# Kernel optimization log

Measured on AMD Instinct MI355X. Metric: run time of the kernel, lower is better.

The kernel has to match this reference:

```python
import jax, jax.numpy as jnp
import numpy as np

D = 768   # embedding_dimensions (richness) — hardcoded in source
H = 3     # heads — hardcoded in source


def setup_inputs() -> dict:
    key = jax.random.key(0)
    ks = jax.random.split(key, 12)
    s = 1.0 / np.sqrt(D)
    s3 = 1.0 / np.sqrt(H * D)
    return {
        "x": jax.random.normal(ks[0], (4, 2048, D), dtype=jnp.float32),
        # QKV projections: Linear(D, D*H), stored as (in, out)
        "Wq": jax.random.uniform(ks[1], (D, D * H), jnp.float32, -s, s),
        "bq": jax.random.uniform(ks[2], (D * H,), jnp.float32, -s, s),
        "Wk": jax.random.uniform(ks[3], (D, D * H), jnp.float32, -s, s),
        "bk": jax.random.uniform(ks[4], (D * H,), jnp.float32, -s, s),
        "Wv": jax.random.uniform(ks[5], (D, D * H), jnp.float32, -s, s),
        "bv": jax.random.uniform(ks[6], (D * H,), jnp.float32, -s, s),
        # final projection: Linear(H*D, D)
        "Wo": jax.random.uniform(ks[7], (H * D, D), jnp.float32, -s3, s3),
        "bo": jax.random.uniform(ks[8], (D,), jnp.float32, -s3, s3),
        # FFN: Linear(D, D) + LeakyReLU
        "Wf": jax.random.uniform(ks[9], (D, D), jnp.float32, -s, s),
        "bf": jax.random.uniform(ks[10], (D,), jnp.float32, -s, s),
    }


def reference(x, Wq, bq, Wk, bk, Wv, bv, Wo, bo, Wf, bf):
    B, S, _ = x.shape
    # QKV: [B,S,H*D] -> [B,H,S,D]  (head dim == full D, as in source)
    q = (x @ Wq + bq).reshape(B, S, H, D).transpose(0, 2, 1, 3)
    k = (x @ Wk + bk).reshape(B, S, H, D).transpose(0, 2, 1, 3)
    v = (x @ Wv + bv).reshape(B, S, H, D).transpose(0, 2, 1, 3)
    # unscaled attention scores (source applies no 1/sqrt(d))
    scores = jnp.einsum('bhqd,bhkd->bhqk', q, k)
    # faithful masking: tril of the scores themselves, fill zeros with -99999
    masked = jnp.where(jnp.tril(scores) == 0, jnp.float32(-99999.0), scores)
    attn = jax.nn.softmax(masked, axis=-1)
    o = jnp.einsum('bhqk,bhkd->bhqd', attn, v)
    o = o.transpose(0, 2, 1, 3).reshape(B, S, H * D)
    a = o @ Wo + bo
    # "normalisation": subtract global mean over the whole tensor
    n = a - jnp.mean(a)
    y = n + x  # residual
    return jax.nn.leaky_relu(y @ Wf + bf, negative_slope=0.01)
```

## Files before the change

kernel.cpp:

```cpp
#include <hip/hip_runtime.h>
#include <hip/hip_bf16.h>

typedef __attribute__((ext_vector_type(8))) __bf16 bf16x8;
typedef __attribute__((ext_vector_type(4))) float f32x4;
typedef unsigned short u16;

#define DEV static __device__ __forceinline__

#define BAR() asm volatile("s_barrier" ::: "memory")
#define LGKM0() asm volatile("s_waitcnt lgkmcnt(0)" ::: "memory")
#define VMCNT6() asm volatile("s_waitcnt vmcnt(6)" ::: "memory")
#define VMCNT3() asm volatile("s_waitcnt vmcnt(3)" ::: "memory")
#define VMCNT0() asm volatile("s_waitcnt vmcnt(0)" ::: "memory")

DEV void load_lds16(const void* g, void* l) {
  __builtin_amdgcn_global_load_lds(
      (const __attribute__((address_space(1))) unsigned int*)g,
      (__attribute__((address_space(3))) unsigned int*)l, 16, 0, 0);
}

DEV u16 bf16bits(float v) {
  __hip_bfloat16 h = __float2bfloat16(v);
  return __builtin_bit_cast(u16, h);
}

DEV bf16x8 rdfrag(const u16* region, int row, int ks, int l) {
  const int cb = (((ks << 6) | ((l >> 4) << 4)) ^ ((l & 7) << 4));
  return *(const bf16x8*)((const char*)region + row * 128 + cb);
}

DEV bf16x8 rdfrag32(const u16* region, int row, int l) {
  const int cb = (((l >> 4) ^ ((row >> 1) & 3)) << 4);
  return *(const bf16x8*)((const char*)region + row * 64 + cb);
}

struct OffN { unsigned long long a[12], b[12], c[12]; };

enum { G128_SC = 0, G128_PV = 1, G128_PLAIN = 2, G128_LEAKY = 3 };

__global__ __launch_bounds__(512, 1) void k_qkv256(
    const u16* __restrict__ A, const u16* __restrict__ B,
    const float* __restrict__ bias, u16* __restrict__ C, u16* __restrict__ Vt)
{
  int flat = blockIdx.y * 27 + blockIdx.x;
  flat = (flat & 7) * 108 + (flat >> 3);
  const int n0 = (flat % 27) * 256, m0 = (flat / 27) * 256;
  const int lda = 768, ldb = 768, nkt = 12;

  __shared__ u16 smem[65536];

  const int tid = threadIdx.x;
  const int l = tid & 63;
  const int wid = tid >> 6;
  const int wm = wid >> 1, wn = wid & 1;

  const int r0s = wid * 16 + (l >> 3);
  const int ces = ((l & 7) ^ (l >> 3)) << 3;
  const size_t aR0 = (size_t)(m0 + r0s) * lda + ces;
  const size_t aR1 = aR0 + (size_t)8 * lda;
  const size_t bR0 = (size_t)(n0 + r0s) * ldb + ces;
  const size_t bR1 = bR0 + (size_t)8 * ldb;
  const size_t hA = (size_t)128 * lda, hB = (size_t)128 * ldb;
  const int dst0 = wid * 1024 + l * 8, dst1 = dst0 + 512;
  u16* As0 = smem;
  u16* Bs0 = smem + 32768;

#define STAGE_A(bf, h, kkv) do {                                 \
    u16* Lp = As0 + (bf) * 16384 + (h) * 8192;                   \
    load_lds16(A + aR0 + ((h) ? hA : 0) + (kkv), Lp + dst0);     \
    load_lds16(A + aR1 + ((h) ? hA : 0) + (kkv), Lp + dst1);     \
  } while (0)
#define STAGE_B(bf, h, kkv) do {                                 \
    u16* Lp = Bs0 + (bf) * 16384 + (h) * 8192;                   \
    load_lds16(B + bR0 + ((h) ? hB : 0) + (kkv), Lp + dst0);     \
    load_lds16(B + bR1 + ((h) ? hB : 0) + (kkv), Lp + dst1);     \
  } while (0)

  f32x4 acc[2][2][2][4] = {};
  bf16x8 af[2][2], bA[4][2], bB[4][2];

#define MFMA16(QM, QN, BARR)                                                  \
    __builtin_amdgcn_s_setprio(1);                                            \
    _Pragma("unroll") for (int ks = 0; ks < 2; ks++)                          \
      _Pragma("unroll") for (int fm = 0; fm < 2; fm++)                        \
        _Pragma("unroll") for (int fn = 0; fn < 4; fn++)                      \
          acc[QM][QN][fm][fn] = __builtin_amdgcn_mfma_f32_16x16x32_bf16(      \
              af[fm][ks], BARR[fn][ks], acc[QM][QN][fm][fn], 0, 0, 0);        \
    __builtin_amdgcn_s_setprio(0);

#define RD_A(half)                                                            \
    _Pragma("unroll") for (int fm = 0; fm < 2; fm++)                          \
      _Pragma("unroll") for (int ks = 0; ks < 2; ks++)                        \
        af[fm][ks] = rdfrag(half, wm * 32 + fm * 16 + (l & 15), ks, l);
#define RD_B(dstv, half)                                                      \
    _Pragma("unroll") for (int fn = 0; fn < 4; fn++)                          \
      _Pragma("unroll") for (int ks = 0; ks < 2; ks++)                        \
        dstv[fn][ks] = rdfrag(half, wn * 64 + fn * 16 + (l & 15), ks, l);

  STAGE_A(0, 0, 0); STAGE_B(0, 0, 0); STAGE_B(0, 1, 0); STAGE_A(0, 1, 0);
  STAGE_A(1, 0, 64); STAGE_B(1, 0, 64); STAGE_B(1, 1, 64);
  VMCNT6();
  BAR();

  for (int t = 0; t < nkt; ++t) {
    const int cur = t & 1, nxt = cur ^ 1;
    const int kk1 = (t + 1) << 6, kk2 = (t + 2) << 6;
    const bool s1 = (t + 1 < nkt), s2 = (t + 2 < nkt);
    RD_A(As0 + cur * 16384);
    RD_B(bA, Bs0 + cur * 16384);
    if (s1) STAGE_A(nxt, 1, kk1);
    BAR();
    MFMA16(0, 0, bA);
    BAR();
    RD_B(bB, Bs0 + cur * 16384 + 8192);
    if (s2) STAGE_A(cur, 0, kk2);
    BAR();
    MFMA16(0, 1, bB);
    BAR();
    RD_A(As0 + cur * 16384 + 8192);
    if (s2) STAGE_B(cur, 0, kk2);
    BAR();
    MFMA16(1, 1, bB);
    BAR();
    if (s2) STAGE_B(cur, 1, kk2);
    BAR();
    MFMA16(1, 0, bA);
    if (s2) { VMCNT6(); } else { VMCNT0(); }
    BAR();
  }
#undef RD_A
#undef RD_B
#undef MFMA16
#undef STAGE_A
#undef STAGE_B

  __syncthreads();
  const int sel = n0 >= 4608 ? 2 : (n0 >= 2304 ? 1 : 0);
  const int r0c = (l >> 4) << 2;
  if (sel == 2) {
#pragma unroll
    for (int Qm = 0; Qm < 2; Qm++)
#pragma unroll
      for (int Qn = 0; Qn < 2; Qn++)
#pragma unroll
        for (int fn = 0; fn < 4; fn++) {
          const int coll = Qn * 128 + wn * 64 + fn * 16 + (l & 15);
          const float bv = bias[n0 + coll];
#pragma unroll
          for (int fm = 0; fm < 2; fm++)
#pragma unroll
            for (int r = 0; r < 4; r++) {
              const int rowl = Qm * 128 + wm * 32 + fm * 16 + r0c + r;
              smem[coll * 256 + ((((rowl >> 3) ^ (coll & 7)) << 3) | (rowl & 7))] =
                  bf16bits(acc[Qm][Qn][fm][fn][r] + bv);
            }
        }
    __syncthreads();
    const int n0v = n0 - 4608;
    const int h = n0v / 768, d0l = n0v % 768;
    const int b = m0 >> 11, sbase = m0 & 2047;
    u16* Cb = Vt + ((size_t)(b * 3 + h) * 768 + d0l) * 2048 + sbase;
#pragma unroll
    for (int j = 0; j < 16; j++) {
      const int dr = j * 16 + (tid >> 5);
      const int c8 = tid & 31;
      bf16x8 v = *(const bf16x8*)&smem[dr * 256 + ((c8 ^ (dr & 7)) << 3)];
      *(bf16x8*)&Cb[(size_t)dr * 2048 + c8 * 8] = v;
    }
  } else {
#pragma unroll
    for (int Qm = 0; Qm < 2; Qm++)
#pragma unroll
      for (int Qn = 0; Qn < 2; Qn++)
#pragma unroll
        for (int fn = 0; fn < 4; fn++) {
          const int coll = Qn * 128 + wn * 64 + fn * 16 + (l & 15);
          const float bv = bias[n0 + coll];
#pragma unroll
          for (int fm = 0; fm < 2; fm++)
#pragma unroll
            for (int r = 0; r < 4; r++) {
              const int rowl = Qm * 128 + wm * 32 + fm * 16 + r0c + r;
              smem[rowl * 256 + (coll ^ (((rowl >> 2) & 3) << 4))] =
                  bf16bits(acc[Qm][Qn][fm][fn][r] + bv);
            }
        }
    __syncthreads();
    u16* Cb = C + (size_t)sel * (8192ull * 2304) + (n0 - sel * 2304);
#pragma unroll
    for (int j = 0; j < 16; j++) {
      const int rowl = j * 16 + (tid >> 5);
      const int c = (tid & 31) * 8;
      bf16x8 v = *(const bf16x8*)&smem[rowl * 256 + (c ^ (((rowl >> 2) & 3) << 4))];
      *(bf16x8*)&Cb[(size_t)(m0 + rowl) * 2304 + c] = v;
    }
  }
}

template<int MODE>
__global__ __launch_bounds__(512, 4) void k_g128(
    const u16* __restrict__ Abase, const u16* __restrict__ Bbase,
    const float* __restrict__ bias, void* __restrict__ Cbase,
    float* __restrict__ part,
    long lda, long ldb, long ldc, int K, OffN off)
{
  int m0, n0, z, r = 0, rb = 0, nkt, arow0, brow0;
  const u16 *A, *B;
  if (MODE == G128_SC) {
    r = blockIdx.y; z = blockIdx.z;
    rb = r >> 1;
    if ((int)blockIdx.x > rb) return;
    m0 = r * 128; n0 = blockIdx.x * 256;
    nkt = K >> 5;
    A = Abase + off.a[z]; B = Bbase + off.b[z];
    arow0 = m0; brow0 = n0;
  } else if (MODE == G128_PV) {
    r = 15 - (int)blockIdx.y;
    rb = r >> 1;
    z = blockIdx.x / 3;
    m0 = r * 128; n0 = (blockIdx.x % 3) * 256;
    nkt = (rb + 1) * 8;
    lda = (long)(rb + 1) * 256;
    A = Abase + off.a[z] + (size_t)32768 * rb * (rb + 1);
    B = Bbase + off.b[z];
    arow0 = (r & 1) * 128; brow0 = n0;
  } else {
    z = 0;
    m0 = blockIdx.y * 128; n0 = blockIdx.x * 256;
    nkt = K >> 5;
    A = Abase; B = Bbase;
    arow0 = m0; brow0 = n0;
  }

  __shared__ u16 smem[39168];

  const int tid = threadIdx.x;
  const int l = tid & 63;
  const int wid = tid >> 6;
  const int wm = wid & 1;
  const int wn = wid >> 1;

  const int ces = (((tid & 3) ^ ((tid >> 3) & 3)) << 3);
  const u16* aS  = A + (size_t)(arow0 + (tid >> 2)) * lda + ces;
  const u16* bS0 = B + (size_t)(brow0 + (tid >> 2)) * ldb + ces;
  const u16* bS1 = bS0 + (size_t)128 * ldb;
  const int t8 = tid * 8;

#define STG(buf, kkv) do {                         \
    u16* Lp = smem + (buf) * 12288;                \
    load_lds16(aS + (kkv), Lp + t8);               \
    load_lds16(bS0 + (kkv), Lp + 4096 + t8);       \
    load_lds16(bS1 + (kkv), Lp + 8192 + t8);       \
  } while (0)

  float* ftab = (float*)(smem + 36864);
  if (MODE == G128_PV) {
    if (tid < 128) {
      const float2* pp = (const float2*)part + (size_t)z * 16384 + (m0 + tid);
      float m = -1e30f;
      for (int t = 0; t <= rb; t++) m = fmaxf(m, pp[(size_t)t * 2048].x);
      float den = 0.f;
      for (int t = 0; t <= rb; t++) {
        const float2 q = pp[(size_t)t * 2048];
        const float e = __expf(q.x - m);
        den += q.y * e;
        ftab[tid * 9 + t] = e;
      }
      ftab[tid * 9 + 8] = 1.f / den;
    }
    LGKM0();
  }

  f32x4 acc[4][4] = {};
  bf16x8 af[4], bf[4];

  STG(0, 0);
  STG(1, 32);
  VMCNT3();
  BAR();

  for (int t = 0; t < nkt; ++t) {
    const u16* Ar = smem + (t % 3) * 12288;
    const u16* Br = Ar + 4096;
#pragma unroll
    for (int fm = 0; fm < 4; fm++)
      af[fm] = rdfrag32(Ar, wm * 64 + fm * 16 + (l & 15), l);
#pragma unroll
    for (int fn = 0; fn < 4; fn++)
      bf[fn] = rdfrag32(Br, wn * 64 + fn * 16 + (l & 15), l);
    if (MODE == G128_PV) {
      const int tcol = t >> 3;
#pragma unroll
      for (int fm = 0; fm < 4; fm++) {
        const int row = wm * 64 + fm * 16 + (l & 15);
        const float ft = ftab[row * 9 + tcol];
#pragma unroll
        for (int i = 0; i < 8; i++)
          af[fm][i] = (__bf16)((float)af[fm][i] * ft);
      }
    }
    const bool s2 = (t + 2 < nkt);
    if (s2) STG((t + 2) % 3, (t + 2) << 5);
    __builtin_amdgcn_s_setprio(1);
#pragma unroll
    for (int fm = 0; fm < 4; fm++)
#pragma unroll
      for (int fn = 0; fn < 4; fn++)
        acc[fm][fn] = __builtin_amdgcn_mfma_f32_16x16x32_bf16(
            af[fm], bf[fn], acc[fm][fn], 0, 0, 0);
    __builtin_amdgcn_s_setprio(0);
    if (s2) { VMCNT3(); } else if (t + 1 < nkt) { VMCNT0(); }
    BAR();
  }
#undef STG

  const int r0c = (l >> 4) << 2;
  if (MODE == G128_SC) {
    float mx4[4][4], s4[4][4];
#pragma unroll
    for (int fm = 0; fm < 4; fm++)
#pragma unroll
      for (int rr = 0; rr < 4; rr++) {
        const int gi = m0 + wm * 64 + fm * 16 + r0c + rr;
        float mv = -1e30f;
#pragma unroll
        for (int fn = 0; fn < 4; fn++) {
          const int gc = n0 + wn * 64 + fn * 16 + (l & 15);
          float v = (gc <= gi) ? acc[fm][fn][rr] : -1e30f;
          acc[fm][fn][rr] = v;
          mv = fmaxf(mv, v);
        }
        mx4[fm][rr] = mv;
      }
#pragma unroll
    for (int o = 1; o < 16; o <<= 1)
#pragma unroll
      for (int fm = 0; fm < 4; fm++)
#pragma unroll
        for (int rr = 0; rr < 4; rr++)
          mx4[fm][rr] = fmaxf(mx4[fm][rr], __shfl_xor(mx4[fm][rr], o, 64));
    float* redm = (float*)smem;
    float* reds = redm + 512;
#pragma unroll
    for (int fm = 0; fm < 4; fm++)
#pragma unroll
      for (int rr = 0; rr < 4; rr++)
        if ((l & 15) == fm * 4 + rr)
          redm[(wm * 64 + fm * 16 + r0c + rr) * 4 + wn] = mx4[fm][rr];
    __syncthreads();
#pragma unroll
    for (int fm = 0; fm < 4; fm++)
#pragma unroll
      for (int rr = 0; rr < 4; rr++) {
        const int rowl = wm * 64 + fm * 16 + r0c + rr;
        f32x4 rm = *(const f32x4*)&redm[rowl * 4];
        const float tm = fmaxf(fmaxf(rm[0], rm[1]), fmaxf(rm[2], rm[3]));
        float ss = 0.f;
#pragma unroll
        for (int fn = 0; fn < 4; fn++) {
          const float e = __expf(acc[fm][fn][rr] - tm);
          acc[fm][fn][rr] = e;
          ss += e;
        }
        s4[fm][rr] = ss;
      }
#pragma unroll
    for (int o = 1; o < 16; o <<= 1)
#pragma unroll
      for (int fm = 0; fm < 4; fm++)
#pragma unroll
        for (int rr = 0; rr < 4; rr++)
          s4[fm][rr] += __shfl_xor(s4[fm][rr], o, 64);
#pragma unroll
    for (int fm = 0; fm < 4; fm++)
#pragma unroll
      for (int rr = 0; rr < 4; rr++)
        if ((l & 15) == fm * 4 + rr)
          reds[(wm * 64 + fm * 16 + r0c + rr) * 4 + wn] = s4[fm][rr];
    __syncthreads();
    if (tid < 128) {
      f32x4 rm = *(const f32x4*)&redm[tid * 4];
      f32x4 rs = *(const f32x4*)&reds[tid * 4];
      float2 pw;
      pw.x = fmaxf(fmaxf(rm[0], rm[1]), fmaxf(rm[2], rm[3]));
      pw.y = rs[0] + rs[1] + rs[2] + rs[3];
      ((float2*)part)[((size_t)z * 8 + blockIdx.x) * 2048 + m0 + tid] = pw;
    }
    __syncthreads();
#pragma unroll
    for (int fn = 0; fn < 4; fn++) {
      const int coll = wn * 64 + fn * 16 + (l & 15);
#pragma unroll
      for (int fm = 0; fm < 4; fm++)
#pragma unroll
        for (int rr = 0; rr < 4; rr++) {
          const int rowl = wm * 64 + fm * 16 + r0c + rr;
          smem[rowl * 256 + (coll ^ (((rowl >> 2) & 3) << 4))] =
              bf16bits(acc[fm][fn][rr]);
        }
    }
    __syncthreads();
    u16* Cb = (u16*)Cbase + off.c[z] + (size_t)32768 * rb * (rb + 1);
    const int W = (rb + 1) << 8;
    const int pr0 = (r & 1) * 128;
#pragma unroll
    for (int j = 0; j < 8; j++) {
      const int rowl = j * 16 + (tid >> 5);
      const int c = (tid & 31) * 8;
      bf16x8 v = *(const bf16x8*)&smem[rowl * 256 + (c ^ (((rowl >> 2) & 3) << 4))];
      *(bf16x8*)&Cb[(size_t)(pr0 + rowl) * W + n0 + c] = v;
    }
  } else if (MODE == G128_PV) {
    __syncthreads();
#pragma unroll
    for (int fn = 0; fn < 4; fn++) {
      const int coll = wn * 64 + fn * 16 + (l & 15);
#pragma unroll
      for (int fm = 0; fm < 4; fm++)
#pragma unroll
        for (int rr = 0; rr < 4; rr++) {
          const int rowl = wm * 64 + fm * 16 + r0c + rr;
          smem[rowl * 256 + (coll ^ (((rowl >> 2) & 3) << 4))] =
              bf16bits(acc[fm][fn][rr] * ftab[rowl * 9 + 8]);
        }
    }
    __syncthreads();
    u16* Cb = (u16*)Cbase + off.c[z] + n0;
#pragma unroll
    for (int j = 0; j < 8; j++) {
      const int rowl = j * 16 + (tid >> 5);
      const int c = (tid & 31) * 8;
      bf16x8 v = *(const bf16x8*)&smem[rowl * 256 + (c ^ (((rowl >> 2) & 3) << 4))];
      *(bf16x8*)&Cb[(size_t)(m0 + rowl) * 2304 + c] = v;
    }
  } else {
#pragma unroll
    for (int fn = 0; fn < 4; fn++) {
      const int col = n0 + wn * 64 + fn * 16 + (l & 15);
      const float bv = bias[col];
#pragma unroll
      for (int fm = 0; fm < 4; fm++)
#pragma unroll
        for (int rr = 0; rr < 4; rr++) {
          const int rowl = wm * 64 + fm * 16 + r0c + rr;
          float v = acc[fm][fn][rr] + bv;
          if (MODE == G128_LEAKY) v = v > 0.f ? v : 0.01f * v;
          ((float*)Cbase)[(size_t)(m0 + rowl) * ldc + col] = v;
        }
    }
  }
}

__global__ __launch_bounds__(256) void k_cast_x(const float* __restrict__ in,
                                                u16* __restrict__ out) {
  const size_t i = ((size_t)blockIdx.x * 256 + threadIdx.x) * 4;
  float4 v = *(const float4*)&in[i];
  ushort4 o;
  o.x = bf16bits(v.x); o.y = bf16bits(v.y); o.z = bf16bits(v.z); o.w = bf16bits(v.w);
  *(ushort4*)&out[i] = o;
}

__global__ __launch_bounds__(256) void k_wt3(const float* __restrict__ w0,
                                             const float* __restrict__ w1,
                                             const float* __restrict__ w2,
                                             u16* __restrict__ out) {
  const float* in = blockIdx.z == 0 ? w0 : (blockIdx.z == 1 ? w1 : w2);
  u16* o = out + (size_t)blockIdx.z * 2304 * 768;
  __shared__ float tile[32][33];
  const int c0 = blockIdx.x * 32, r0 = blockIdx.y * 32;
  const int tx = threadIdx.x, ty = threadIdx.y;
#pragma unroll
  for (int k = 0; k < 4; k++)
    tile[ty + 8 * k][tx] = in[(size_t)(r0 + ty + 8 * k) * 2304 + c0 + tx];
  __syncthreads();
#pragma unroll
  for (int k = 0; k < 4; k++)
    o[(size_t)(c0 + ty + 8 * k) * 768 + r0 + tx] = bf16bits(tile[tx][ty + 8 * k]);
}

__global__ __launch_bounds__(256) void k_wt(const float* __restrict__ in,
                                            u16* __restrict__ out, int R, int C) {
  __shared__ float tile[32][33];
  const int c0 = blockIdx.x * 32, r0 = blockIdx.y * 32;
  const int tx = threadIdx.x, ty = threadIdx.y;
#pragma unroll
  for (int k = 0; k < 4; k++)
    tile[ty + 8 * k][tx] = in[(size_t)(r0 + ty + 8 * k) * C + c0 + tx];
  __syncthreads();
#pragma unroll
  for (int k = 0; k < 4; k++)
    out[(size_t)(c0 + ty + 8 * k) * R + r0 + tx] = bf16bits(tile[tx][ty + 8 * k]);
}

__global__ __launch_bounds__(256) void k_bias_concat(const float* __restrict__ bq,
                                                     const float* __restrict__ bk,
                                                     const float* __restrict__ bv,
                                                     float* __restrict__ out) {
  const int i = blockIdx.x * 256 + threadIdx.x;
  if (i < 2304) out[i] = bq[i];
  else if (i < 4608) out[i] = bk[i - 2304];
  else if (i < 6912) out[i] = bv[i - 4608];
}

__global__ __launch_bounds__(256) void k_red1(const float* __restrict__ a,
                                              float* __restrict__ part) {
  float s = 0.f;
  for (size_t idx = (size_t)blockIdx.x * 256 + threadIdx.x; idx < 6291456ull; idx += 2048ull * 256)
    s += a[idx];
#pragma unroll
  for (int o = 32; o >= 1; o >>= 1) s += __shfl_xor(s, o, 64);
  __shared__ float r[4];
  const int t = threadIdx.x, w = t >> 6;
  if ((t & 63) == 0) r[w] = s;
  __syncthreads();
  if (t == 0) part[blockIdx.x] = r[0] + r[1] + r[2] + r[3];
}

__global__ __launch_bounds__(256) void k_red2(const float* __restrict__ part,
                                              float* __restrict__ mean) {
  const int t = threadIdx.x;
  float s = 0.f;
  for (int i = t; i < 2048; i += 256) s += part[i];
#pragma unroll
  for (int o = 32; o >= 1; o >>= 1) s += __shfl_xor(s, o, 64);
  __shared__ float r[4];
  const int w = t >> 6;
  if ((t & 63) == 0) r[w] = s;
  __syncthreads();
  if (t == 0) mean[0] = (r[0] + r[1] + r[2] + r[3]) * (1.f / 6291456.f);
}

__global__ __launch_bounds__(256) void k_residual(const float* __restrict__ a,
                                                  const float* __restrict__ x,
                                                  const float* __restrict__ meanp,
                                                  u16* __restrict__ yb) {
  const float mean = meanp[0];
  const size_t i = ((size_t)blockIdx.x * 256 + threadIdx.x) * 4;
  float4 av = *(const float4*)&a[i];
  float4 xv = *(const float4*)&x[i];
  ushort4 o;
  o.x = bf16bits(av.x - mean + xv.x);
  o.y = bf16bits(av.y - mean + xv.y);
  o.z = bf16bits(av.z - mean + xv.z);
  o.w = bf16bits(av.w - mean + xv.w);
  *(ushort4*)&yb[i] = o;
}

extern "C" void kernel_launch(void* const* d_in, const int* in_sizes, int n_in,
                              void* d_out, int out_size, void* d_ws, size_t ws_size,
                              hipStream_t stream) {
  const float* x   = (const float*)d_in[0];
  const float* Wq  = (const float*)d_in[1];
  const float* bq  = (const float*)d_in[2];
  const float* Wk  = (const float*)d_in[3];
  const float* bk  = (const float*)d_in[4];
  const float* Wv  = (const float*)d_in[5];
  const float* bv  = (const float*)d_in[6];
  const float* Wo  = (const float*)d_in[7];
  const float* bo  = (const float*)d_in[8];
  const float* Wf  = (const float*)d_in[9];
  const float* bfb = (const float*)d_in[10];

  char* ws = (char*)d_ws;
  const size_t MSZ    = 37748736;
  const size_t o_Wqkvt = 0;
  const size_t o_Wot  = 10616832;
  const size_t o_Wft  = o_Wot + 3538944;
  const size_t o_bqkv = o_Wft + 1179648;
  const size_t o_prt  = o_bqkv + 32768;
  const size_t o_mn   = o_prt + 8192;
  const size_t o_part = o_mn + 256;
  const size_t o_xb   = o_part + 1572864;
  const size_t o_Q    = o_xb + 12582912;
  const size_t o_K    = o_Q + MSZ;
  const size_t o_Vt   = o_K + MSZ;
  const size_t o_P    = o_Vt + MSZ;
  const size_t o_end  = o_P + 56623104;
  if (ws_size < o_end) return;

  const size_t o_O  = o_Q;
  const size_t o_a  = o_K;
  const size_t o_yb = o_xb;

  OffN z0{};
  dim3 b32(32, 8);

  k_cast_x<<<6144, 256, 0, stream>>>(x, (u16*)(ws + o_xb));
  k_wt3<<<dim3(72, 24, 3), b32, 0, stream>>>(Wq, Wk, Wv, (u16*)(ws + o_Wqkvt));
  k_wt<<<dim3(24, 72), b32, 0, stream>>>(Wo, (u16*)(ws + o_Wot), 2304, 768);
  k_wt<<<dim3(24, 24), b32, 0, stream>>>(Wf, (u16*)(ws + o_Wft), 768, 768);
  k_bias_concat<<<27, 256, 0, stream>>>(bq, bk, bv, (float*)(ws + o_bqkv));

  k_qkv256<<<dim3(27, 32), 512, 0, stream>>>(
      (const u16*)(ws + o_xb), (const u16*)(ws + o_Wqkvt),
      (const float*)(ws + o_bqkv), (u16*)(ws + o_Q), (u16*)(ws + o_Vt));

  OffN so{}, po{};
  for (int zz = 0; zz < 12; zz++) {
    const int b = zz / 3, h = zz % 3;
    so.a[zz] = (size_t)b * 2048 * 2304 + (size_t)h * 768;
    so.b[zz] = so.a[zz];
    so.c[zz] = (size_t)zz * 2359296;
    po.a[zz] = so.c[zz];
    po.b[zz] = (size_t)zz * 768 * 2048;
    po.c[zz] = so.a[zz];
  }
  k_g128<G128_SC><<<dim3(8, 16, 12), 512, 0, stream>>>(
      (const u16*)(ws + o_Q), (const u16*)(ws + o_K), nullptr, ws + o_P,
      (float*)(ws + o_part), 2304, 2304, 0, 768, so);
  k_g128<G128_PV><<<dim3(36, 16), 512, 0, stream>>>(
      (const u16*)(ws + o_P), (const u16*)(ws + o_Vt), nullptr, ws + o_O,
      (float*)(ws + o_part), 0, 2048, 0, 0, po);

  k_g128<G128_PLAIN><<<dim3(3, 64), 512, 0, stream>>>(
      (const u16*)(ws + o_O), (const u16*)(ws + o_Wot), bo, ws + o_a,
      nullptr, 2304, 2304, 768, 2304, z0);

  k_red1<<<2048, 256, 0, stream>>>((const float*)(ws + o_a), (float*)(ws + o_prt));
  k_red2<<<1, 256, 0, stream>>>((const float*)(ws + o_prt), (float*)(ws + o_mn));
  k_residual<<<6144, 256, 0, stream>>>((const float*)(ws + o_a), x,
                                       (const float*)(ws + o_mn), (u16*)(ws + o_yb));

  k_g128<G128_LEAKY><<<dim3(3, 64), 512, 0, stream>>>(
      (const u16*)(ws + o_yb), (const u16*)(ws + o_Wft), bfb, d_out,
      nullptr, 768, 768, 768, 768, z0);
}
```

Baseline: 374.7 us.

## Fold global mean subtraction into FFN bias and fuse residual into Wo epilogue

```diff
diff --git a/kernel.cpp b/kernel.cpp
--- a/kernel.cpp
+++ b/kernel.cpp
@@ -36,7 +36,7 @@
 
 struct OffN { unsigned long long a[12], b[12], c[12]; };
 
-enum { G128_SC = 0, G128_PV = 1, G128_PLAIN = 2, G128_LEAKY = 3 };
+enum { G128_SC = 0, G128_PV = 1, G128_WO = 2, G128_LEAKY = 3 };
 
 __global__ __launch_bounds__(512, 1) void k_qkv256(
     const u16* __restrict__ A, const u16* __restrict__ B,
@@ -201,13 +201,14 @@
 __global__ __launch_bounds__(512, 4) void k_g128(
     const u16* __restrict__ Abase, const u16* __restrict__ Bbase,
     const float* __restrict__ bias, void* __restrict__ Cbase,
-    float* __restrict__ part,
+    float* __restrict__ part, const float* __restrict__ xin,
     long lda, long ldb, long ldc, int K, OffN off)
 {
   int m0, n0, z, r = 0, rb = 0, nkt, arow0, brow0;
   const u16 *A, *B;
   if (MODE == G128_SC) {
-    r = blockIdx.y; z = blockIdx.z;
+    r = 15 - (int)blockIdx.y;
+    z = blockIdx.z;
     rb = r >> 1;
     if ((int)blockIdx.x > rb) return;
     m0 = r * 128; n0 = blockIdx.x * 256;
@@ -433,6 +434,43 @@
       bf16x8 v = *(const bf16x8*)&smem[rowl * 256 + (c ^ (((rowl >> 2) & 3) << 4))];
       *(bf16x8*)&Cb[(size_t)(m0 + rowl) * 2304 + c] = v;
     }
+  } else if (MODE == G128_WO) {
+    float lsum = 0.f;
+    __syncthreads();
+#pragma unroll
+    for (int fn = 0; fn < 4; fn++) {
+      const int coll = wn * 64 + fn * 16 + (l & 15);
+      const float bv = bias[n0 + coll];
+#pragma unroll
+      for (int fm = 0; fm < 4; fm++)
+#pragma unroll
+        for (int rr = 0; rr < 4; rr++) {
+          const int rowl = wm * 64 + fm * 16 + r0c + rr;
+          const float a_val = acc[fm][fn][rr] + bv;
+          lsum += a_val;
+          const float y = a_val + xin[(size_t)(m0 + rowl) * 768 + n0 + coll];
+          smem[rowl * 256 + (coll ^ (((rowl >> 2) & 3) << 4))] = bf16bits(y);
+        }
+    }
+#pragma unroll
+    for (int o = 32; o >= 1; o >>= 1) lsum += __shfl_xor(lsum, o, 64);
+    float* red = (float*)(smem + 32768);
+    if (l == 0) red[wid] = lsum;
+    __syncthreads();
+    if (tid == 0) {
+      float s = 0.f;
+#pragma unroll
+      for (int i = 0; i < 8; i++) s += red[i];
+      part[blockIdx.y * 3 + blockIdx.x] = s;
+    }
+    u16* Cb = (u16*)Cbase + n0;
+#pragma unroll
+    for (int j = 0; j < 8; j++) {
+      const int rowl = j * 16 + (tid >> 5);
+      const int c = (tid & 31) * 8;
+      bf16x8 v = *(const bf16x8*)&smem[rowl * 256 + (c ^ (((rowl >> 2) & 3) << 4))];
+      *(bf16x8*)&Cb[(size_t)(m0 + rowl) * ldc + c] = v;
+    }
   } else {
 #pragma unroll
     for (int fn = 0; fn < 4; fn++) {
@@ -444,7 +482,7 @@
         for (int rr = 0; rr < 4; rr++) {
           const int rowl = wm * 64 + fm * 16 + r0c + rr;
           float v = acc[fm][fn][rr] + bv;
-          if (MODE == G128_LEAKY) v = v > 0.f ? v : 0.01f * v;
+          v = v > 0.f ? v : 0.01f * v;
           ((float*)Cbase)[(size_t)(m0 + rowl) * ldc + col] = v;
         }
     }
@@ -502,25 +540,10 @@
   else if (i < 6912) out[i] = bv[i - 4608];
 }
 
-__global__ __launch_bounds__(256) void k_red1(const float* __restrict__ a,
-                                              float* __restrict__ part) {
-  float s = 0.f;
-  for (size_t idx = (size_t)blockIdx.x * 256 + threadIdx.x; idx < 6291456ull; idx += 2048ull * 256)
-    s += a[idx];
-#pragma unroll
-  for (int o = 32; o >= 1; o >>= 1) s += __shfl_xor(s, o, 64);
-  __shared__ float r[4];
-  const int t = threadIdx.x, w = t >> 6;
-  if ((t & 63) == 0) r[w] = s;
-  __syncthreads();
-  if (t == 0) part[blockIdx.x] = r[0] + r[1] + r[2] + r[3];
-}
-
-__global__ __launch_bounds__(256) void k_red2(const float* __restrict__ part,
+__global__ __launch_bounds__(256) void k_mean(const float* __restrict__ part,
                                               float* __restrict__ mean) {
   const int t = threadIdx.x;
-  float s = 0.f;
-  for (int i = t; i < 2048; i += 256) s += part[i];
+  float s = (t < 192) ? part[t] : 0.f;
 #pragma unroll
   for (int o = 32; o >= 1; o >>= 1) s += __shfl_xor(s, o, 64);
   __shared__ float r[4];
@@ -530,20 +553,14 @@
   if (t == 0) mean[0] = (r[0] + r[1] + r[2] + r[3]) * (1.f / 6291456.f);
 }
 
-__global__ __launch_bounds__(256) void k_residual(const float* __restrict__ a,
-                                                  const float* __restrict__ x,
-                                                  const float* __restrict__ meanp,
-                                                  u16* __restrict__ yb) {
-  const float mean = meanp[0];
-  const size_t i = ((size_t)blockIdx.x * 256 + threadIdx.x) * 4;
-  float4 av = *(const float4*)&a[i];
-  float4 xv = *(const float4*)&x[i];
-  ushort4 o;
-  o.x = bf16bits(av.x - mean + xv.x);
-  o.y = bf16bits(av.y - mean + xv.y);
-  o.z = bf16bits(av.z - mean + xv.z);
-  o.w = bf16bits(av.w - mean + xv.w);
-  *(ushort4*)&yb[i] = o;
+__global__ __launch_bounds__(256) void k_ffbias(const float* __restrict__ Wf,
+                                                const float* __restrict__ bfb,
+                                                const float* __restrict__ meanp,
+                                                float* __restrict__ out) {
+  const int j = blockIdx.x * 256 + threadIdx.x;
+  float s = 0.f;
+  for (int k = 0; k < 768; k++) s += Wf[(size_t)k * 768 + j];
+  out[j] = bfb[j] - meanp[0] * s;
 }
 
 extern "C" void kernel_launch(void* const* d_in, const int* in_sizes, int n_in,
@@ -569,7 +586,8 @@
   const size_t o_bqkv = o_Wft + 1179648;
   const size_t o_prt  = o_bqkv + 32768;
   const size_t o_mn   = o_prt + 8192;
-  const size_t o_part = o_mn + 256;
+  const size_t o_bff  = o_mn + 256;
+  const size_t o_part = o_bff + 4096;
   const size_t o_xb   = o_part + 1572864;
   const size_t o_Q    = o_xb + 12582912;
   const size_t o_K    = o_Q + MSZ;
@@ -579,7 +597,6 @@
   if (ws_size < o_end) return;
 
   const size_t o_O  = o_Q;
-  const size_t o_a  = o_K;
   const size_t o_yb = o_xb;
 
   OffN z0{};
@@ -607,21 +624,21 @@
   }
   k_g128<G128_SC><<<dim3(8, 16, 12), 512, 0, stream>>>(
       (const u16*)(ws + o_Q), (const u16*)(ws + o_K), nullptr, ws + o_P,
-      (float*)(ws + o_part), 2304, 2304, 0, 768, so);
+      (float*)(ws + o_part), nullptr, 2304, 2304, 0, 768, so);
   k_g128<G128_PV><<<dim3(36, 16), 512, 0, stream>>>(
       (const u16*)(ws + o_P), (const u16*)(ws + o_Vt), nullptr, ws + o_O,
-      (float*)(ws + o_part), 0, 2048, 0, 0, po);
-
-  k_g128<G128_PLAIN><<<dim3(3, 64), 512, 0, stream>>>(
-      (const u16*)(ws + o_O), (const u16*)(ws + o_Wot), bo, ws + o_a,
-      nullptr, 2304, 2304, 768, 2304, z0);
-
-  k_red1<<<2048, 256, 0, stream>>>((const float*)(ws + o_a), (float*)(ws + o_prt));
-  k_red2<<<1, 256, 0, stream>>>((const float*)(ws + o_prt), (float*)(ws + o_mn));
-  k_residual<<<6144, 256, 0, stream>>>((const float*)(ws + o_a), x,
-                                       (const float*)(ws + o_mn), (u16*)(ws + o_yb));
+      (float*)(ws + o_part), nullptr, 0, 2048, 0, 0, po);
+
+  k_g128<G128_WO><<<dim3(3, 64), 512, 0, stream>>>(
+      (const u16*)(ws + o_O), (const u16*)(ws + o_Wot), bo, ws + o_yb,
+      (float*)(ws + o_prt), x, 2304, 2304, 768, 2304, z0);
+
+  k_mean<<<1, 256, 0, stream>>>((const float*)(ws + o_prt), (float*)(ws + o_mn));
+  k_ffbias<<<3, 256, 0, stream>>>(Wf, bfb, (const float*)(ws + o_mn),
+                                  (float*)(ws + o_bff));
 
   k_g128<G128_LEAKY><<<dim3(3, 64), 512, 0, stream>>>(
-      (const u16*)(ws + o_yb), (const u16*)(ws + o_Wft), bfb, d_out,
-      nullptr, 768, 768, 768, 768, z0);
-}
+      (const u16*)(ws + o_yb), (const u16*)(ws + o_Wft),
+      (const float*)(ws + o_bff), d_out,
+      nullptr, nullptr, 768, 768, 768, 768, z0);
+}
```

After: 388.3 us. 3.6% more time.
